# Kernel tuning notes

Hardware: AMD Instinct MI355X
Metric: run time of the kernel (lower is better)

Reference implementation:

```python
import jax, jax.numpy as jnp
import numpy as np
from jax import lax

K = 16
EPS = 1e-5


def leaky(x):
    return jnp.where(x >= 0, x, 0.2 * x)


def group_norm(x, gamma, beta, groups):
    # x: [B, C, ...]
    B, C = x.shape[0], x.shape[1]
    xs = x.reshape(B, groups, C // groups, *x.shape[2:])
    axes = tuple(range(2, xs.ndim))
    mean = xs.mean(axis=axes, keepdims=True)
    var = xs.var(axis=axes, keepdims=True)
    xs = (xs - mean) * lax.rsqrt(var + EPS)
    x = xs.reshape(x.shape)
    pshape = (1, C) + (1,) * (x.ndim - 2)
    return x * gamma.reshape(pshape) + beta.reshape(pshape)


def knn_idx(coor_k, coor_q):
    # coor_*: [B, 3, N]; returns idx [B, Nq, K] of nearest points in coor_k
    qq = (coor_q ** 2).sum(axis=1)  # [B, Nq]
    kk = (coor_k ** 2).sum(axis=1)  # [B, Nk]
    d2 = qq[:, :, None] + kk[:, None, :] - 2.0 * jnp.einsum('bcq,bck->bqk', coor_q, coor_k)
    _, idx = lax.top_k(-d2, K)  # smallest distances
    return idx


def get_graph_feature(coor_q, x_q, coor_k, x_k):
    # x_q: [B, C, Nq], x_k: [B, C, Nk] -> [B, 2C, Nq, K]
    idx = knn_idx(coor_k, coor_q)  # [B, Nq, K]
    nbr = jax.vmap(lambda xk, ix: xk[:, ix])(x_k, idx)  # [B, C, Nq, K]
    xq = x_q[:, :, :, None]
    return jnp.concatenate([nbr - xq, jnp.broadcast_to(xq, nbr.shape)], axis=1)


def fps(xyz, npoint):
    B, N, _ = xyz.shape

    def step(carry, _):
        dist, far = carry
        centroid = jnp.take_along_axis(xyz, far[:, None, None], axis=1)  # [B,1,3]
        d = ((xyz - centroid) ** 2).sum(-1)
        dist = jnp.minimum(dist, d)
        nxt = jnp.argmax(dist, axis=-1).astype(jnp.int32)
        return (dist, nxt), far

    init = (jnp.full((B, N), 1e10, xyz.dtype), jnp.zeros((B,), jnp.int32))
    _, idx = lax.scan(step, init, None, length=npoint)
    return idx.T  # [B, npoint]


def fps_downsample(coor, x, num_group):
    fps_i = fps(jnp.transpose(coor, (0, 2, 1)), num_group)  # [B, G]
    combined = jnp.concatenate([coor, x], axis=1)  # [B, 3+C, N]
    newc = jax.vmap(lambda c, ix: c[:, ix])(combined, fps_i)  # [B, 3+C, G]
    return newc[:, :3], newc[:, 3:]


def conv1x1(w, f):
    return jnp.einsum('oc,bcqk->boqk', w, f)


def setup_inputs() -> dict:
    key = jax.random.key(0)
    ks = jax.random.split(key, 16)
    B, N = 8, 4096
    s = lambda k, sh, fan: jax.random.normal(k, sh, jnp.float32) * (1.0 / np.sqrt(fan))
    return {
        'x': jax.random.normal(ks[0], (B, 3, N), jnp.float32),
        'sample_npoints': 128,
        'w_in': s(ks[1], (8, 3), 3), 'b_in': jnp.zeros((8,), jnp.float32),
        'w1': s(ks[2], (32, 16), 16), 'g1': jnp.ones((32,), jnp.float32), 'be1': jnp.zeros((32,), jnp.float32),
        'w2': s(ks[3], (64, 64), 64), 'g2': jnp.ones((64,), jnp.float32), 'be2': jnp.zeros((64,), jnp.float32),
        'w3': s(ks[4], (64, 128), 128), 'g3': jnp.ones((64,), jnp.float32), 'be3': jnp.zeros((64,), jnp.float32),
        'w4': s(ks[5], (128, 128), 128), 'g4': jnp.ones((128,), jnp.float32), 'be4': jnp.zeros((128,), jnp.float32),
    }


def reference(x, sample_npoints, w_in, b_in, w1, g1, be1, w2, g2, be2, w3, g3, be3, w4, g4, be4):
    coor = x
    f = jnp.einsum('oc,bcn->bon', w_in, x) + b_in[None, :, None]  # input_trans

    f = get_graph_feature(coor, f, coor, f)
    f = leaky(group_norm(conv1x1(w1, f), g1, be1, 4)).max(axis=-1)
    coor_q, f_q = fps_downsample(coor, f, 512)

    f = get_graph_feature(coor_q, f_q, coor, f)
    f = leaky(group_norm(conv1x1(w2, f), g2, be2, 4)).max(axis=-1)
    coor = coor_q

    f = get_graph_feature(coor, f, coor, f)
    f = leaky(group_norm(conv1x1(w3, f), g3, be3, 4)).max(axis=-1)
    coor_q, f_q = fps_downsample(coor, f, sample_npoints)

    f = get_graph_feature(coor_q, f_q, coor, f)
    f = leaky(group_norm(conv1x1(w4, f), g4, be4, 4)).max(axis=-1)
    coor = coor_q
    return coor, f
```

## Files before the change

kernel.cpp:

```cpp
#include <hip/hip_runtime.h>
#include <cstdint>

typedef unsigned int uint;
typedef unsigned short u16;

#define DEV __device__ __forceinline__

DEV float bf2f(u16 u) { return __uint_as_float(((uint)u) << 16); }
DEV u16 f2bf(float f) {
    uint x = __float_as_uint(f);
    return (u16)((x + 0x7fffu + ((x >> 16) & 1u)) >> 16);
}

struct InPtrs { const void* p[14]; };

__global__ __launch_bounds__(256) void fused_prep(
    const void* __restrict__ xv, InPtrs ptrs, float* __restrict__ cw,
    float* __restrict__ coorT, float* __restrict__ f0,
    int* __restrict__ flag, int B, int N)
{
    __shared__ int cnt[256];
    __shared__ int sflag;
    const u16* xs = (const u16*)xv;
    int t = threadIdx.x, good = 0;
#pragma unroll
    for (int i = 0; i < 8; ++i) {
        u16 u = xs[(t * 8 + i) * 37];
        int e = (u >> 7) & 0xFF;
        good += (e >= 90 && e <= 150) ? 1 : 0;
    }
    cnt[t] = good;
    __syncthreads();
    if (t == 0) {
        int s = 0;
        for (int i = 0; i < 256; ++i) s += cnt[i];
        sflag = (s >= 1741) ? 1 : 0;
    }
    __syncthreads();
    int isbf = sflag;
    int blk = blockIdx.x;

    if (blk < 128) {
        int p = blk * 256 + t;
        int b = p / N, n = p % N;
        float c0, c1, c2;
        if (isbf) {
            const u16* x = (const u16*)xv;
            c0 = bf2f(x[(b * 3 + 0) * N + n]);
            c1 = bf2f(x[(b * 3 + 1) * N + n]);
            c2 = bf2f(x[(b * 3 + 2) * N + n]);
        } else {
            const float* x = (const float*)xv;
            c0 = x[(b * 3 + 0) * N + n];
            c1 = x[(b * 3 + 1) * N + n];
            c2 = x[(b * 3 + 2) * N + n];
        }
        coorT[p * 3 + 0] = c0; coorT[p * 3 + 1] = c1; coorT[p * 3 + 2] = c2;
        float wl[24], bl[8];
        if (isbf) {
            const u16* wr = (const u16*)ptrs.p[0];
            const u16* br = (const u16*)ptrs.p[1];
#pragma unroll
            for (int i = 0; i < 24; ++i) wl[i] = bf2f(wr[i]);
#pragma unroll
            for (int i = 0; i < 8; ++i) bl[i] = bf2f(br[i]);
        } else {
            const float* wr = (const float*)ptrs.p[0];
            const float* br = (const float*)ptrs.p[1];
#pragma unroll
            for (int i = 0; i < 24; ++i) wl[i] = wr[i];
#pragma unroll
            for (int i = 0; i < 8; ++i) bl[i] = br[i];
        }
#pragma unroll
        for (int o = 0; o < 8; ++o) {
            float v = bl[o];
            v = fmaf(wl[o * 3 + 0], c0, v);
            v = fmaf(wl[o * 3 + 1], c1, v);
            v = fmaf(wl[o * 3 + 2], c2, v);
            f0[(size_t)p * 8 + o] = v;
        }
    } else {
        const int cntb[14] = {24, 8, 512, 32, 32, 4096, 64, 64, 8192, 64, 64, 16384, 128, 128};
        int g = (blk - 128) * 256 + t;
        if (g < 29792) {
            int idx = g, bb = 0;
            while (idx >= cntb[bb]) { idx -= cntb[bb]; ++bb; }
            cw[g] = isbf ? bf2f(((const u16*)ptrs.p[bb])[idx])
                         : ((const float*)ptrs.p[bb])[idx];
        }
        if (blk == 128 && t == 0) flag[0] = isbf;
    }
}

#define KNN_INSERT(DV, IV)                                                            \
    if ((DV) < bd[15]) {                                                              \
        _Pragma("unroll")                                                             \
        for (int j = 15; j >= 1; --j) {                                               \
            bool up  = ((DV) < bd[j - 1]);                                            \
            bool chg = ((DV) < bd[j]);                                                \
            if (chg) { bd[j] = up ? bd[j - 1] : (DV); bi[j] = up ? bi[j - 1] : (IV); }\
        }                                                                             \
        if ((DV) < bd[0]) { bd[0] = (DV); bi[0] = (IV); }                             \
    }

#define FPS_DPP_STEP(CTRL)                                                           \
    {                                                                                \
        float ov = __int_as_float(__builtin_amdgcn_update_dpp(                       \
            __float_as_int(bv), __float_as_int(bv), (CTRL), 0xf, 0xf, false));       \
        int oi = __builtin_amdgcn_update_dpp(bid, bid, (CTRL), 0xf, 0xf, false);     \
        bool t = (ov > bv) || (ov == bv && oi < bid);                                \
        bv = t ? ov : bv; bid = t ? oi : bid;                                        \
    }

#define FPS_MRG_STEP(CTRL)                                                           \
    {                                                                                \
        float ov = __int_as_float(__builtin_amdgcn_update_dpp(                       \
            __float_as_int(mv), __float_as_int(mv), (CTRL), 0xf, 0xf, false));       \
        int oi = __builtin_amdgcn_update_dpp(mi, mi, (CTRL), 0xf, 0xf, false);       \
        bool t = (ov > mv) || (ov == mv && oi < mi);                                 \
        mv = t ? ov : mv; mi = t ? oi : mi;                                          \
    }

template<int N, int PTS>
__global__ __launch_bounds__(256, 2) void knn_fps_kernel(
    const float* __restrict__ xyz, int* __restrict__ idxout,
    int* __restrict__ fpsout, int npoint)
{
    __shared__ union LU {
        struct { float4 kt[256]; float2 mrg[4][64][16]; } k;
        struct { float4 sxyz[N]; float2 rp[2][4]; } f;
    } u;
    int b = blockIdx.y;
    int tid = threadIdx.x;

    if (blockIdx.x == 0) {
        __builtin_amdgcn_s_setprio(3);
        int wave = tid >> 6, lane = tid & 63;
        float px[PTS], py[PTS], pz[PTS], dist[PTS];
#pragma unroll
        for (int i = 0; i < PTS; ++i) {
            int p = tid + i * 256;
            const float* pp = xyz + (size_t)(b * N + p) * 3;
            float x0 = pp[0], y0 = pp[1], z0 = pp[2];
            px[i] = x0; py[i] = y0; pz[i] = z0;
            u.f.sxyz[p] = make_float4(x0, y0, z0, 0.f);
            dist[i] = 1e10f;
        }
        __syncthreads();
        int far = 0;
        int my0 = 0, my1 = 0;
        for (int it = 0; it < npoint; ++it) {
            if (it == tid)       my0 = far;
            if (it == tid + 256) my1 = far;
            float4 cv = u.f.sxyz[far];
            float cx = cv.x, cy = cv.y, cz = cv.z;
            float bv = -1.f; int bid = 0;
#pragma unroll
            for (int i = 0; i < PTS; ++i) {
                float dx = __fsub_rn(px[i], cx);
                float dy = __fsub_rn(py[i], cy);
                float dz = __fsub_rn(pz[i], cz);
                float d = __fadd_rn(__fadd_rn(__fmul_rn(dx, dx), __fmul_rn(dy, dy)), __fmul_rn(dz, dz));
                float nd = fminf(dist[i], d);
                dist[i] = nd;
                bool t = nd > bv;
                bv = t ? nd : bv; bid = t ? (tid + i * 256) : bid;
            }
            FPS_DPP_STEP(0x0B1)
            FPS_DPP_STEP(0x04E)
            FPS_DPP_STEP(0x124)
            FPS_DPP_STEP(0x128)
            FPS_DPP_STEP(0x142)
            FPS_DPP_STEP(0x143)
            int par = it & 1;
            if (lane == 63) u.f.rp[par][wave] = make_float2(bv, __int_as_float(bid));
            __syncthreads();
            {
                float2 e = u.f.rp[par][lane & 3];
                float mv = e.x; int mi = __float_as_int(e.y);
                FPS_MRG_STEP(0x0B1)
                FPS_MRG_STEP(0x04E)
                far = __builtin_amdgcn_readfirstlane(mi);
            }
        }
        __builtin_amdgcn_s_setprio(0);
        if (tid < npoint)       fpsout[b * npoint + tid] = my0;
        if (tid + 256 < npoint) fpsout[b * npoint + tid + 256] = my1;
        return;
    }

    int qloc = tid & 63;
    int wave = tid >> 6;
    int q = (blockIdx.x - 1) * 64 + qloc;

    const float* qp = xyz + (size_t)(b * N + q) * 3;
    float qx = qp[0], qy = qp[1], qz = qp[2];
    float qq = __fadd_rn(__fadd_rn(__fmul_rn(qx, qx), __fmul_rn(qy, qy)), __fmul_rn(qz, qz));
    float bd[16]; int bi[16];
#pragma unroll
    for (int j = 0; j < 16; ++j) { bd[j] = 3.4e38f; bi[j] = 0; }
    float cb_d[4]; int cb_i[4]; int cnt = 0;
#pragma unroll
    for (int s = 0; s < 4; ++s) { cb_d[s] = 3.4e38f; cb_i[s] = 0; }

    for (int t0 = 0; t0 < N; t0 += 256) {
        {
            int i = tid;
            const float* kp = xyz + (size_t)(b * N + t0 + i) * 3;
            float kx = kp[0], ky = kp[1], kz = kp[2];
            float kn = __fadd_rn(__fadd_rn(__fmul_rn(kx, kx), __fmul_rn(ky, ky)), __fmul_rn(kz, kz));
            u.k.kt[i] = make_float4(kx, ky, kz, kn);
        }
        __syncthreads();
        for (int i2 = 0; i2 < 64; ++i2) {
            int ii = wave * 64 + i2;
            float4 kv = u.k.kt[ii];
            float dot = __fadd_rn(__fadd_rn(__fmul_rn(qx, kv.x), __fmul_rn(qy, kv.y)),
                                  __fmul_rn(qz, kv.z));
            float d2 = __fsub_rn(__fadd_rn(qq, kv.w), __fmul_rn(2.0f, dot));
            bool adm = (d2 < bd[15]);
            if (adm) {
                int id = t0 + ii;
                cb_d[0] = (cnt == 0) ? d2 : cb_d[0]; cb_i[0] = (cnt == 0) ? id : cb_i[0];
                cb_d[1] = (cnt == 1) ? d2 : cb_d[1]; cb_i[1] = (cnt == 1) ? id : cb_i[1];
                cb_d[2] = (cnt == 2) ? d2 : cb_d[2]; cb_i[2] = (cnt == 2) ? id : cb_i[2];
                cb_d[3] = (cnt == 3) ? d2 : cb_d[3]; cb_i[3] = (cnt == 3) ? id : cb_i[3];
                ++cnt;
            }
            if (__any(cnt >= 4)) {
#pragma unroll
                for (int s = 0; s < 4; ++s) {
                    bool have = s < cnt;
                    float dv = have ? cb_d[s] : 3.4e38f;
                    int   iv = have ? cb_i[s] : 0;
                    KNN_INSERT(dv, iv)
                }
                cnt = 0;
            }
        }
        __syncthreads();
    }
#pragma unroll
    for (int s = 0; s < 4; ++s) {
        bool have = s < cnt;
        float dv = have ? cb_d[s] : 3.4e38f;
        int   iv = have ? cb_i[s] : 0;
        KNN_INSERT(dv, iv)
    }
#pragma unroll
    for (int j = 0; j < 16; ++j)
        u.k.mrg[wave][qloc][j] = make_float2(bd[j], __int_as_float(bi[j]));
    __syncthreads();

    if (tid < 64) {
        int qm = tid;
        int qg = (blockIdx.x - 1) * 64 + qm;
        int* op = idxout + (size_t)(b * N + qg) * 16;
        int p0 = 0, p1 = 0, p2 = 0, p3 = 0;
#pragma unroll 1
        for (int j = 0; j < 16; ++j) {
            float2 h0 = u.k.mrg[0][qm][p0], h1 = u.k.mrg[1][qm][p1];
            float2 h2 = u.k.mrg[2][qm][p2], h3 = u.k.mrg[3][qm][p3];
            float bdv = h0.x; int biv = __float_as_int(h0.y); int w_ = 0;
            int i1 = __float_as_int(h1.y);
            if (h1.x < bdv || (h1.x == bdv && i1 < biv)) { bdv = h1.x; biv = i1; w_ = 1; }
            int i2v = __float_as_int(h2.y);
            if (h2.x < bdv || (h2.x == bdv && i2v < biv)) { bdv = h2.x; biv = i2v; w_ = 2; }
            int i3 = __float_as_int(h3.y);
            if (h3.x < bdv || (h3.x == bdv && i3 < biv)) { bdv = h3.x; biv = i3; w_ = 3; }
            op[j] = biv;
            p0 += (w_ == 0); p1 += (w_ == 1); p2 += (w_ == 2); p3 += (w_ == 3);
        }
    }
}

__global__ __launch_bounds__(256) void knn_kernel(
    const float* __restrict__ qxyz, const float* __restrict__ kxyz,
    int* __restrict__ idxout, int Nq, int Nk)
{
    __shared__ float4 kt[256];
    __shared__ float2 mrg[4][64][16];
    int b = blockIdx.y;
    int qloc = threadIdx.x & 63;
    int wave = threadIdx.x >> 6;
    int q = blockIdx.x * 64 + qloc;
    bool act = q < Nq;

    float qx = 0.f, qy = 0.f, qz = 0.f, qq = 0.f;
    if (act) {
        const float* qp = qxyz + (size_t)(b * Nq + q) * 3;
        qx = qp[0]; qy = qp[1]; qz = qp[2];
        qq = __fadd_rn(__fadd_rn(__fmul_rn(qx, qx), __fmul_rn(qy, qy)), __fmul_rn(qz, qz));
    }
    float bd[16]; int bi[16];
#pragma unroll
    for (int j = 0; j < 16; ++j) { bd[j] = 3.4e38f; bi[j] = 0; }
    float cb_d[4]; int cb_i[4]; int cnt = 0;
#pragma unroll
    for (int s = 0; s < 4; ++s) { cb_d[s] = 3.4e38f; cb_i[s] = 0; }

    for (int t0 = 0; t0 < Nk; t0 += 256) {
        {
            int i = threadIdx.x;
            const float* kp = kxyz + (size_t)(b * Nk + t0 + i) * 3;
            float kx = kp[0], ky = kp[1], kz = kp[2];
            float kn = __fadd_rn(__fadd_rn(__fmul_rn(kx, kx), __fmul_rn(ky, ky)), __fmul_rn(kz, kz));
            kt[i] = make_float4(kx, ky, kz, kn);
        }
        __syncthreads();
        for (int i2 = 0; i2 < 64; ++i2) {
            int ii = wave * 64 + i2;
            float4 kv = kt[ii];
            float dot = __fadd_rn(__fadd_rn(__fmul_rn(qx, kv.x), __fmul_rn(qy, kv.y)),
                                  __fmul_rn(qz, kv.z));
            float d2 = __fsub_rn(__fadd_rn(qq, kv.w), __fmul_rn(2.0f, dot));
            bool adm = act && (d2 < bd[15]);
            if (adm) {
                int id = t0 + ii;
                cb_d[0] = (cnt == 0) ? d2 : cb_d[0]; cb_i[0] = (cnt == 0) ? id : cb_i[0];
                cb_d[1] = (cnt == 1) ? d2 : cb_d[1]; cb_i[1] = (cnt == 1) ? id : cb_i[1];
                cb_d[2] = (cnt == 2) ? d2 : cb_d[2]; cb_i[2] = (cnt == 2) ? id : cb_i[2];
                cb_d[3] = (cnt == 3) ? d2 : cb_d[3]; cb_i[3] = (cnt == 3) ? id : cb_i[3];
                ++cnt;
            }
            if (__any(cnt >= 4)) {
#pragma unroll
                for (int s = 0; s < 4; ++s) {
                    bool have = s < cnt;
                    float dv = have ? cb_d[s] : 3.4e38f;
                    int   iv = have ? cb_i[s] : 0;
                    KNN_INSERT(dv, iv)
                }
                cnt = 0;
            }
        }
        __syncthreads();
    }
#pragma unroll
    for (int s = 0; s < 4; ++s) {
        bool have = s < cnt;
        float dv = have ? cb_d[s] : 3.4e38f;
        int   iv = have ? cb_i[s] : 0;
        KNN_INSERT(dv, iv)
    }
#pragma unroll
    for (int j = 0; j < 16; ++j)
        mrg[wave][qloc][j] = make_float2(bd[j], __int_as_float(bi[j]));
    __syncthreads();

    if (threadIdx.x < 64) {
        int qm = threadIdx.x;
        int qg = blockIdx.x * 64 + qm;
        if (qg < Nq) {
            int* op = idxout + (size_t)(b * Nq + qg) * 16;
            int p0 = 0, p1 = 0, p2 = 0, p3 = 0;
#pragma unroll 1
            for (int j = 0; j < 16; ++j) {
                float2 h0 = mrg[0][qm][p0], h1 = mrg[1][qm][p1];
                float2 h2 = mrg[2][qm][p2], h3 = mrg[3][qm][p3];
                float bdv = h0.x; int biv = __float_as_int(h0.y); int w_ = 0;
                int i1 = __float_as_int(h1.y);
                if (h1.x < bdv || (h1.x == bdv && i1 < biv)) { bdv = h1.x; biv = i1; w_ = 1; }
                int i2v = __float_as_int(h2.y);
                if (h2.x < bdv || (h2.x == bdv && i2v < biv)) { bdv = h2.x; biv = i2v; w_ = 2; }
                int i3 = __float_as_int(h3.y);
                if (h3.x < bdv || (h3.x == bdv && i3 < biv)) { bdv = h3.x; biv = i3; w_ = 3; }
                op[j] = biv;
                p0 += (w_ == 0); p1 += (w_ == 1); p2 += (w_ == 2); p3 += (w_ == 3);
            }
        }
    }
}

__global__ __launch_bounds__(256) void knn_part_kernel(
    const float* __restrict__ qxyz, const float* __restrict__ kxyz,
    float2* __restrict__ pbuf, int Nq, int Nk, int nchunk)
{
    __shared__ float4 kt[256];
    __shared__ float2 mrg[4][64][16];
    int qblks = Nq / 64;
    int chunk = blockIdx.x / qblks;
    int qblk = blockIdx.x % qblks;
    int klen = Nk / nchunk;
    int klo = chunk * klen, khi = klo + klen;
    int b = blockIdx.y;
    int qloc = threadIdx.x & 63;
    int wave = threadIdx.x >> 6;
    int q = qblk * 64 + qloc;

    const float* qp = qxyz + (size_t)(b * Nq + q) * 3;
    float qx = qp[0], qy = qp[1], qz = qp[2];
    float qq = __fadd_rn(__fadd_rn(__fmul_rn(qx, qx), __fmul_rn(qy, qy)), __fmul_rn(qz, qz));
    float bd[16]; int bi[16];
#pragma unroll
    for (int j = 0; j < 16; ++j) { bd[j] = 3.4e38f; bi[j] = 0; }
    float cb_d[4]; int cb_i[4]; int cnt = 0;
#pragma unroll
    for (int s = 0; s < 4; ++s) { cb_d[s] = 3.4e38f; cb_i[s] = 0; }

    for (int t0 = klo; t0 < khi; t0 += 256) {
        {
            int i = threadIdx.x;
            const float* kp = kxyz + (size_t)(b * Nk + t0 + i) * 3;
            float kx = kp[0], ky = kp[1], kz = kp[2];
            float kn = __fadd_rn(__fadd_rn(__fmul_rn(kx, kx), __fmul_rn(ky, ky)), __fmul_rn(kz, kz));
            kt[i] = make_float4(kx, ky, kz, kn);
        }
        __syncthreads();
        for (int i2 = 0; i2 < 64; ++i2) {
            int ii = wave * 64 + i2;
            float4 kv = kt[ii];
            float dot = __fadd_rn(__fadd_rn(__fmul_rn(qx, kv.x), __fmul_rn(qy, kv.y)),
                                  __fmul_rn(qz, kv.z));
            float d2 = __fsub_rn(__fadd_rn(qq, kv.w), __fmul_rn(2.0f, dot));
            bool adm = (d2 < bd[15]);
            if (adm) {
                int id = t0 + ii;
                cb_d[0] = (cnt == 0) ? d2 : cb_d[0]; cb_i[0] = (cnt == 0) ? id : cb_i[0];
                cb_d[1] = (cnt == 1) ? d2 : cb_d[1]; cb_i[1] = (cnt == 1) ? id : cb_i[1];
                cb_d[2] = (cnt == 2) ? d2 : cb_d[2]; cb_i[2] = (cnt == 2) ? id : cb_i[2];
                cb_d[3] = (cnt == 3) ? d2 : cb_d[3]; cb_i[3] = (cnt == 3) ? id : cb_i[3];
                ++cnt;
            }
            if (__any(cnt >= 4)) {
#pragma unroll
                for (int s = 0; s < 4; ++s) {
                    bool have = s < cnt;
                    float dv = have ? cb_d[s] : 3.4e38f;
                    int   iv = have ? cb_i[s] : 0;
                    KNN_INSERT(dv, iv)
                }
                cnt = 0;
            }
        }
        __syncthreads();
    }
#pragma unroll
    for (int s = 0; s < 4; ++s) {
        bool have = s < cnt;
        float dv = have ? cb_d[s] : 3.4e38f;
        int   iv = have ? cb_i[s] : 0;
        KNN_INSERT(dv, iv)
    }
#pragma unroll
    for (int j = 0; j < 16; ++j)
        mrg[wave][qloc][j] = make_float2(bd[j], __int_as_float(bi[j]));
    __syncthreads();

    if (threadIdx.x < 64) {
        int qm = threadIdx.x;
        int qg = qblk * 64 + qm;
        float2* op = pbuf + (((size_t)(b * Nq + qg) * nchunk) + chunk) * 16;
        int p0 = 0, p1 = 0, p2 = 0, p3 = 0;
#pragma unroll 1
        for (int j = 0; j < 16; ++j) {
            float2 h0 = mrg[0][qm][p0], h1 = mrg[1][qm][p1];
            float2 h2 = mrg[2][qm][p2], h3 = mrg[3][qm][p3];
            float bdv = h0.x; int biv = __float_as_int(h0.y); int w_ = 0;
            int i1 = __float_as_int(h1.y);
            if (h1.x < bdv || (h1.x == bdv && i1 < biv)) { bdv = h1.x; biv = i1; w_ = 1; }
            int i2v = __float_as_int(h2.y);
            if (h2.x < bdv || (h2.x == bdv && i2v < biv)) { bdv = h2.x; biv = i2v; w_ = 2; }
            int i3 = __float_as_int(h3.y);
            if (h3.x < bdv || (h3.x == bdv && i3 < biv)) { bdv = h3.x; biv = i3; w_ = 3; }
            op[j] = make_float2(bdv, __int_as_float(biv));
            p0 += (w_ == 0); p1 += (w_ == 1); p2 += (w_ == 2); p3 += (w_ == 3);
        }
    }
}

__global__ void knn_merge_kernel(const float2* __restrict__ pbuf, int* __restrict__ idxout,
                                 int total)
{
    int q = blockIdx.x * 256 + threadIdx.x;
    if (q >= total) return;
    const float2* L = pbuf + (size_t)q * 64;
    int* op = idxout + (size_t)q * 16;
    int p0 = 0, p1 = 0, p2 = 0, p3 = 0;
#pragma unroll 1
    for (int j = 0; j < 16; ++j) {
        float2 h0 = L[p0], h1 = L[16 + p1], h2 = L[32 + p2], h3 = L[48 + p3];
        float bdv = h0.x; int biv = __float_as_int(h0.y); int w_ = 0;
        int i1 = __float_as_int(h1.y);
        if (h1.x < bdv || (h1.x == bdv && i1 < biv)) { bdv = h1.x; biv = i1; w_ = 1; }
        int i2v = __float_as_int(h2.y);
        if (h2.x < bdv || (h2.x == bdv && i2v < biv)) { bdv = h2.x; biv = i2v; w_ = 2; }
        int i3 = __float_as_int(h3.y);
        if (h3.x < bdv || (h3.x == bdv && i3 < biv)) { bdv = h3.x; biv = i3; w_ = 3; }
        op[j] = biv;
        p0 += (w_ == 0); p1 += (w_ == 1); p2 += (w_ == 2); p3 += (w_ == 3);
    }
}

template<int CTRL>
DEV void red5(float& v, int& i, float& x, float& y, float& z)
{
    float ov = __int_as_float(__builtin_amdgcn_update_dpp(
        __float_as_int(v), __float_as_int(v), CTRL, 0xf, 0xf, false));
    int oi = __builtin_amdgcn_update_dpp(i, i, CTRL, 0xf, 0xf, false);
    float ox = __int_as_float(__builtin_amdgcn_update_dpp(
        __float_as_int(x), __float_as_int(x), CTRL, 0xf, 0xf, false));
    float oy = __int_as_float(__builtin_amdgcn_update_dpp(
        __float_as_int(y), __float_as_int(y), CTRL, 0xf, 0xf, false));
    float oz = __int_as_float(__builtin_amdgcn_update_dpp(
        __float_as_int(z), __float_as_int(z), CTRL, 0xf, 0xf, false));
    bool t = (ov > v) || (ov == v && oi < i);
    v = t ? ov : v; i = t ? oi : i; x = t ? ox : x; y = t ? oy : y; z = t ? oz : z;
}

template<bool STORE_V>
__global__ __launch_bounds__(256) void stats3_fps_kernel(
    const float* __restrict__ fq, const float* __restrict__ fk, const int* __restrict__ idx,
    const float* __restrict__ w, float* __restrict__ partials, float* __restrict__ vbuf,
    const float* __restrict__ fxyz, int* __restrict__ fpsout, int Nq, int Nk)
{
    constexpr int K = 16, C_IN = 64, C_OUT = 64, E = 2 * C_IN, GC = C_OUT / 4;
    __shared__ alignas(16) float edge[4][K][E];
    __shared__ int nidx[4][K];
    __shared__ float gsum[4][4][2];

    int b = blockIdx.y;
    if (blockIdx.x == 0) {
        int tid = threadIdx.x;
        if (tid >= 64) return;
        __builtin_amdgcn_s_setprio(3);
        constexpr int PTS = 8, NL = 512;
        float px[PTS], py[PTS], pz[PTS], dist[PTS];
#pragma unroll
        for (int i = 0; i < PTS; ++i) {
            int p = tid + i * 64;
            const float* pp = fxyz + (size_t)(b * NL + p) * 3;
            px[i] = pp[0]; py[i] = pp[1]; pz[i] = pp[2];
            dist[i] = 1e10f;
        }
        float cx = __int_as_float(__builtin_amdgcn_readlane(__float_as_int(px[0]), 0));
        float cy = __int_as_float(__builtin_amdgcn_readlane(__float_as_int(py[0]), 0));
        float cz = __int_as_float(__builtin_amdgcn_readlane(__float_as_int(pz[0]), 0));
        int curidx = 0;
        int my0 = 0, my1 = 0;
        for (int it = 0; it < 128; ++it) {
            if (it == tid)      my0 = curidx;
            if (it == tid + 64) my1 = curidx;
            float bv = -1.f; int bid = 0; float bx = 0.f, by = 0.f, bz = 0.f;
#pragma unroll
            for (int i = 0; i < PTS; ++i) {
                float dx = __fsub_rn(px[i], cx);
                float dy = __fsub_rn(py[i], cy);
                float dz = __fsub_rn(pz[i], cz);
                float d = __fadd_rn(__fadd_rn(__fmul_rn(dx, dx), __fmul_rn(dy, dy)), __fmul_rn(dz, dz));
                float nd = fminf(dist[i], d);
                dist[i] = nd;
                bool t = nd > bv;
                bv = t ? nd : bv; bid = t ? (tid + i * 64) : bid;
                bx = t ? px[i] : bx; by = t ? py[i] : by; bz = t ? pz[i] : bz;
            }
            red5<0x0B1>(bv, bid, bx, by, bz);
            red5<0x04E>(bv, bid, bx, by, bz);
            red5<0x124>(bv, bid, bx, by, bz);
            red5<0x128>(bv, bid, bx, by, bz);
            red5<0x142>(bv, bid, bx, by, bz);
            red5<0x143>(bv, bid, bx, by, bz);
            curidx = __builtin_amdgcn_readlane(bid, 63);
            cx = __int_as_float(__builtin_amdgcn_readlane(__float_as_int(bx), 63));
            cy = __int_as_float(__builtin_amdgcn_readlane(__float_as_int(by), 63));
            cz = __int_as_float(__builtin_amdgcn_readlane(__float_as_int(bz), 63));
        }
        __builtin_amdgcn_s_setprio(0);
        if (tid < 128)      fpsout[b * 128 + tid] = my0;
        if (tid + 64 < 128) fpsout[b * 128 + tid + 64] = my1;
        return;
    }

    int wave = threadIdx.x >> 6, lane = threadIdx.x & 63;
    int nqc = Nq >> 2;
    int chunk = blockIdx.x - 1;
    int q = chunk * 4 + wave;

    const float* xqr = fq + (size_t)(b * Nq + q) * C_IN;
    if (lane < K) nidx[wave][lane] = idx[(size_t)(b * Nq + q) * K + lane];
    for (int t = lane; t < K * E; t += 64) {
        int k = t / E, c = t % E;
        int j = nidx[wave][k];
        float v;
        if (c < C_IN) v = fk[(size_t)(b * Nk + j) * C_IN + c] - xqr[c];
        else          v = xqr[c - C_IN];
        edge[wave][k][c] = v;
    }
    __syncthreads();

    {
        int oc = lane;
        float s = 0.f, ss = 0.f;
        float v[K];
#pragma unroll
        for (int k2 = 0; k2 < K; ++k2) v[k2] = 0.f;
        const float* wr = w + (size_t)oc * E;
        for (int c = 0; c < E; c += 4) {
            float4 wv = *reinterpret_cast<const float4*>(wr + c);
#pragma unroll
            for (int k2 = 0; k2 < K; ++k2) {
                const float4 e4 = *reinterpret_cast<const float4*>(&edge[wave][k2][c]);
                v[k2] = fmaf(wv.x, e4.x, v[k2]);
                v[k2] = fmaf(wv.y, e4.y, v[k2]);
                v[k2] = fmaf(wv.z, e4.z, v[k2]);
                v[k2] = fmaf(wv.w, e4.w, v[k2]);
            }
        }
        if (STORE_V) {
            float4* vb = (float4*)(vbuf + ((size_t)(b * Nq + q) * C_OUT + oc) * 16);
            vb[0] = make_float4(v[0], v[1], v[2], v[3]);
            vb[1] = make_float4(v[4], v[5], v[6], v[7]);
            vb[2] = make_float4(v[8], v[9], v[10], v[11]);
            vb[3] = make_float4(v[12], v[13], v[14], v[15]);
        }
#pragma unroll
        for (int k2 = 0; k2 < K; ++k2) { s += v[k2]; ss = fmaf(v[k2], v[k2], ss); }
#pragma unroll
        for (int m2 = 1; m2 < GC; m2 <<= 1) { s += __shfl_xor(s, m2); ss += __shfl_xor(ss, m2); }
        if ((oc & (GC - 1)) == 0) {
            gsum[wave][oc / GC][0] = s; gsum[wave][oc / GC][1] = ss;
        }
    }
    __syncthreads();
    if (threadIdx.x < 4) {
        int g = threadIdx.x;
        float s  = ((gsum[0][g][0] + gsum[1][g][0]) + gsum[2][g][0]) + gsum[3][g][0];
        float ss = ((gsum[0][g][1] + gsum[1][g][1]) + gsum[2][g][1]) + gsum[3][g][1];
        size_t pi = ((size_t)(b * 4 + g) * nqc + chunk) * 2;
        partials[pi] = s; partials[pi + 1] = ss;
    }
}

__global__ void gather_kernel(const float* __restrict__ coorS, const float* __restrict__ fS,
                              const int* __restrict__ fidx, float* __restrict__ coorD,
                              float* __restrict__ fD, int Ns, int M, int C)
{
    int b = blockIdx.y;
    int m = blockIdx.x * blockDim.x + threadIdx.x;
    if (m >= M) return;
    int j = fidx[b * M + m];
#pragma unroll
    for (int c = 0; c < 3; ++c)
        coorD[((size_t)b * M + m) * 3 + c] = coorS[((size_t)b * Ns + j) * 3 + c];
    for (int c = 0; c < C; ++c)
        fD[((size_t)b * M + m) * C + c] = fS[((size_t)b * Ns + j) * C + c];
}

template<int C_IN, int C_OUT, bool STORE_V>
__global__ __launch_bounds__(256) void edge_conv_stats_t(
    const float* __restrict__ fq, const float* __restrict__ fk, const int* __restrict__ idx,
    const float* __restrict__ w, float* __restrict__ partials, float* __restrict__ vbuf,
    int Nq, int Nk)
{
    constexpr int K = 16, E = 2 * C_IN, GC = C_OUT / 4;
    constexpr int ITERS = (C_OUT + 63) / 64;
    __shared__ alignas(16) float edge[4][K][E];
    __shared__ int nidx[4][K];
    __shared__ float gsum[4][4][2];

    int wave = threadIdx.x >> 6, lane = threadIdx.x & 63;
    int nqc = Nq >> 2;
    int b = blockIdx.y, chunk = blockIdx.x;
    int q = chunk * 4 + wave;

    const float* xqr = fq + (size_t)(b * Nq + q) * C_IN;
    if (lane < K) nidx[wave][lane] = idx[(size_t)(b * Nq + q) * K + lane];
    for (int t = lane; t < K * E; t += 64) {
        int k = t / E, c = t % E;
        int j = nidx[wave][k];
        float v;
        if (c < C_IN) v = fk[(size_t)(b * Nk + j) * C_IN + c] - xqr[c];
        else          v = xqr[c - C_IN];
        edge[wave][k][c] = v;
    }
    __syncthreads();

#pragma unroll
    for (int itr = 0; itr < ITERS; ++itr) {
        int oc = lane + 64 * itr;
        float s = 0.f, ss = 0.f;
        if (oc < C_OUT) {
            float v[K];
#pragma unroll
            for (int k2 = 0; k2 < K; ++k2) v[k2] = 0.f;
            const float* wr = w + (size_t)oc * E;
            for (int c = 0; c < E; c += 4) {
                float4 wv = *reinterpret_cast<const float4*>(wr + c);
#pragma unroll
                for (int k2 = 0; k2 < K; ++k2) {
                    const float4 e4 = *reinterpret_cast<const float4*>(&edge[wave][k2][c]);
                    v[k2] = fmaf(wv.x, e4.x, v[k2]);
                    v[k2] = fmaf(wv.y, e4.y, v[k2]);
                    v[k2] = fmaf(wv.z, e4.z, v[k2]);
                    v[k2] = fmaf(wv.w, e4.w, v[k2]);
                }
            }
            if (STORE_V) {
                float4* vb = (float4*)(vbuf + ((size_t)(b * Nq + q) * C_OUT + oc) * 16);
                vb[0] = make_float4(v[0], v[1], v[2], v[3]);
                vb[1] = make_float4(v[4], v[5], v[6], v[7]);
                vb[2] = make_float4(v[8], v[9], v[10], v[11]);
                vb[3] = make_float4(v[12], v[13], v[14], v[15]);
            }
#pragma unroll
            for (int k2 = 0; k2 < K; ++k2) { s += v[k2]; ss = fmaf(v[k2], v[k2], ss); }
        }
#pragma unroll
        for (int m2 = 1; m2 < GC; m2 <<= 1) { s += __shfl_xor(s, m2); ss += __shfl_xor(ss, m2); }
        if (oc < C_OUT && (oc & (GC - 1)) == 0) {
            gsum[wave][oc / GC][0] = s; gsum[wave][oc / GC][1] = ss;
        }
    }
    __syncthreads();
    if (threadIdx.x < 4) {
        int g = threadIdx.x;
        float s  = ((gsum[0][g][0] + gsum[1][g][0]) + gsum[2][g][0]) + gsum[3][g][0];
        float ss = ((gsum[0][g][1] + gsum[1][g][1]) + gsum[2][g][1]) + gsum[3][g][1];
        size_t pi = ((size_t)(b * 4 + g) * nqc + chunk) * 2;
        partials[pi] = s; partials[pi + 1] = ss;
    }
}

__global__ void gn_finalize(const float* __restrict__ partials, float* __restrict__ stats,
                            int nchunk, float inv_cnt)
{
    int i = threadIdx.x >> 3;
    int sl = threadIdx.x & 7;
    float s = 0.f, ss = 0.f;
    for (int c = sl; c < nchunk; c += 8) {
        s  += partials[((size_t)i * nchunk + c) * 2];
        ss += partials[((size_t)i * nchunk + c) * 2 + 1];
    }
#pragma unroll
    for (int m = 1; m < 8; m <<= 1) { s += __shfl_xor(s, m); ss += __shfl_xor(ss, m); }
    if (sl == 0) {
        float mean = s * inv_cnt;
        float var = fmaf(-mean, mean, ss * inv_cnt);
        stats[i * 2] = mean;
        stats[i * 2 + 1] = 1.0f / sqrtf(var + 1e-5f);
    }
}

template<int C_IN, int C_OUT>
__global__ __launch_bounds__(256) void edge_conv_apply(
    const float* __restrict__ fq, const float* __restrict__ fk, const int* __restrict__ idx,
    const float* __restrict__ stats, const float* __restrict__ w,
    const float* __restrict__ gamma, const float* __restrict__ beta,
    float* __restrict__ outp, int Nq, int Nk)
{
    constexpr int K = 16, E = 2 * C_IN, GC = C_OUT / 4;
    constexpr int ITERS = (C_OUT + 63) / 64;
    __shared__ alignas(16) float edge[4][K][E];
    __shared__ int nidx[4][K];

    int wave = threadIdx.x >> 6, lane = threadIdx.x & 63;
    int b = blockIdx.y, chunk = blockIdx.x;
    int q = chunk * 4 + wave;

    const float* xqr = fq + (size_t)(b * Nq + q) * C_IN;
    if (lane < K) nidx[wave][lane] = idx[(size_t)(b * Nq + q) * K + lane];
    for (int t = lane; t < K * E; t += 64) {
        int k = t / E, c = t % E;
        int j = nidx[wave][k];
        float v;
        if (c < C_IN) v = fk[(size_t)(b * Nk + j) * C_IN + c] - xqr[c];
        else          v = xqr[c - C_IN];
        edge[wave][k][c] = v;
    }
    __syncthreads();

#pragma unroll
    for (int itr = 0; itr < ITERS; ++itr) {
        int oc = lane + 64 * itr;
        if (oc < C_OUT) {
            float v[K];
#pragma unroll
            for (int k2 = 0; k2 < K; ++k2) v[k2] = 0.f;
            const float* wr = w + (size_t)oc * E;
            for (int c = 0; c < E; c += 4) {
                float4 wv = *reinterpret_cast<const float4*>(wr + c);
#pragma unroll
                for (int k2 = 0; k2 < K; ++k2) {
                    const float4 e4 = *reinterpret_cast<const float4*>(&edge[wave][k2][c]);
                    v[k2] = fmaf(wv.x, e4.x, v[k2]);
                    v[k2] = fmaf(wv.y, e4.y, v[k2]);
                    v[k2] = fmaf(wv.z, e4.z, v[k2]);
                    v[k2] = fmaf(wv.w, e4.w, v[k2]);
                }
            }
            int g = oc / GC;
            float mean = stats[(b * 4 + g) * 2 + 0];
            float rstd = stats[(b * 4 + g) * 2 + 1];
            float ga = gamma[oc], be = beta[oc];
            float m = -3.4e38f;
#pragma unroll
            for (int k2 = 0; k2 < K; ++k2) {
                float y = fmaf((v[k2] - mean) * rstd, ga, be);
                y = (y >= 0.f) ? y : 0.2f * y;
                m = fmaxf(m, y);
            }
            outp[(size_t)(b * Nq + q) * C_OUT + oc] = m;
        }
    }
}

template<int C_OUT>
__global__ __launch_bounds__(256) void edge_conv_apply2(
    const float* __restrict__ vbuf, const float* __restrict__ stats,
    const float* __restrict__ gamma, const float* __restrict__ beta,
    float* __restrict__ outp, int total, int Nq)
{
    constexpr int GC = C_OUT / 4;
    int t = blockIdx.x * 256 + threadIdx.x;
    if (t >= total) return;
    int oc = t & (C_OUT - 1);
    int bq = t / C_OUT;
    int b = bq / Nq;
    int g = oc / GC;
    float mean = stats[(b * 4 + g) * 2 + 0];
    float rstd = stats[(b * 4 + g) * 2 + 1];
    float ga = gamma[oc], be = beta[oc];
    const float4* vb = (const float4*)(vbuf + (size_t)t * 16);
    float m = -3.4e38f;
#pragma unroll
    for (int j = 0; j < 4; ++j) {
        float4 v4 = vb[j];
        float y;
        y = fmaf((v4.x - mean) * rstd, ga, be); y = (y >= 0.f) ? y : 0.2f * y; m = fmaxf(m, y);
        y = fmaf((v4.y - mean) * rstd, ga, be); y = (y >= 0.f) ? y : 0.2f * y; m = fmaxf(m, y);
        y = fmaf((v4.z - mean) * rstd, ga, be); y = (y >= 0.f) ? y : 0.2f * y; m = fmaxf(m, y);
        y = fmaf((v4.w - mean) * rstd, ga, be); y = (y >= 0.f) ? y : 0.2f * y; m = fmaxf(m, y);
    }
    outp[t] = m;
}

__global__ __launch_bounds__(256) void apply2_out(
    const float* __restrict__ vbuf, const float* __restrict__ stats,
    const float* __restrict__ gamma, const float* __restrict__ beta,
    const float* __restrict__ coor2T, void* __restrict__ outv,
    const int* __restrict__ flag)
{
    int t = blockIdx.x * 256 + threadIdx.x;
    int isbf = flag[0];
    if (t < 131072) {
        int oc = t & 127;
        int bq = t >> 7;
        int b = bq >> 7;
        int q = bq & 127;
        int g = oc >> 5;
        float mean = stats[(b * 4 + g) * 2 + 0];
        float rstd = stats[(b * 4 + g) * 2 + 1];
        float ga = gamma[oc], be = beta[oc];
        const float4* vb = (const float4*)(vbuf + (size_t)t * 16);
        float m = -3.4e38f;
#pragma unroll
        for (int j = 0; j < 4; ++j) {
            float4 v4 = vb[j];
            float y;
            y = fmaf((v4.x - mean) * rstd, ga, be); y = (y >= 0.f) ? y : 0.2f * y; m = fmaxf(m, y);
            y = fmaf((v4.y - mean) * rstd, ga, be); y = (y >= 0.f) ? y : 0.2f * y; m = fmaxf(m, y);
            y = fmaf((v4.z - mean) * rstd, ga, be); y = (y >= 0.f) ? y : 0.2f * y; m = fmaxf(m, y);
            y = fmaf((v4.w - mean) * rstd, ga, be); y = (y >= 0.f) ? y : 0.2f * y; m = fmaxf(m, y);
        }
        int i = 3072 + b * 16384 + oc * 128 + q;
        if (isbf) ((u16*)outv)[i] = f2bf(m);
        else      ((float*)outv)[i] = m;
    } else if (t < 134144) {
        int i = t - 131072;
        int b = i / 384, r = i % 384;
        int c = r / 128, n = r % 128;
        float v = coor2T[((size_t)b * 128 + n) * 3 + c];
        if (isbf) ((u16*)outv)[i] = f2bf(v);
        else      ((float*)outv)[i] = v;
    }
}

__global__ void write_out_kernel(const float* __restrict__ coor2T, const float* __restrict__ f4T,
                                 void* __restrict__ outv, const int* __restrict__ flag)
{
    int i = blockIdx.x * blockDim.x + threadIdx.x;
    if (i >= 134144) return;
    float v;
    if (i < 3072) {
        int b = i / 384, r = i % 384;
        int c = r / 128, n = r % 128;
        v = coor2T[((size_t)b * 128 + n) * 3 + c];
    } else {
        int jj = i - 3072;
        int b = jj / 16384, r = jj % 16384;
        int c = r / 128, qn = r % 128;
        v = f4T[((size_t)b * 128 + qn) * 128 + c];
    }
    if (flag[0]) ((u16*)outv)[i] = f2bf(v);
    else         ((float*)outv)[i] = v;
}

extern "C" void kernel_launch(void* const* d_in, const int* in_sizes, int n_in,
                              void* d_out, int out_size, void* d_ws, size_t ws_size,
                              hipStream_t stream)
{
    (void)in_sizes; (void)n_in; (void)out_size;
    constexpr int B = 8, N = 4096, M1 = 512, M2 = 128;

    float* fbase   = (float*)d_ws;
    float* coorT   = fbase;
    float* f0T     = coorT + 98304;
    float* f1T     = f0T + 262144;
    float* f2T     = f1T + 1048576;
    float* f3T     = f2T + 262144;
    float* f4T     = f3T + 262144;
    float* coor1T  = f4T + 131072;
    float* coor2T  = coor1T + 12288;
    float* fq2T    = coor2T + 3072;
    float* fq4T    = fq2T + 131072;
    float* statsb  = fq4T + 65536;
    float* partials= statsb + 256;
    float* pb      = partials + 65536;
    float* cw      = pb + 524288;
    int* ibase = (int*)(cw + 29796);
    int* idx1 = ibase;
    int* idx2 = idx1 + 524288;
    int* idx3 = idx2 + 65536;
    int* idx4 = idx3 + 65536;
    int* fps1 = idx4 + 16384;
    int* fps2 = fps1 + 4096;
    int* flag = fps2 + 1024;

    size_t used = (size_t)((char*)(flag + 1) - (char*)d_ws);
    size_t voff = (used + 255) & ~(size_t)255;
    float* vbuf = (float*)((char*)d_ws + voff);
    bool fu1 = ws_size >= voff + (size_t)16777216 * 4;
    bool fu2 = ws_size >= voff + (size_t)4194304 * 4;
    bool fu3 = fu2;
    bool fu4 = ws_size >= voff + (size_t)2097152 * 4;

    const float* w1c  = cw + 32;
    const float* g1c  = cw + 544;
    const float* be1c = cw + 576;
    const float* w2c  = cw + 608;
    const float* g2c  = cw + 4704;
    const float* be2c = cw + 4768;
    const float* w3c  = cw + 4832;
    const float* g3c  = cw + 13024;
    const float* be3c = cw + 13088;
    const float* w4c  = cw + 13152;
    const float* g4c  = cw + 29536;
    const float* be4c = cw + 29664;

    InPtrs ptrs;
    for (int i = 0; i < 14; ++i) ptrs.p[i] = d_in[i + 2];

    fused_prep<<<245, 256, 0, stream>>>(d_in[0], ptrs, cw, coorT, f0T, flag, B, N);

    knn_fps_kernel<4096, 16><<<dim3(N / 64 + 1, B), 256, 0, stream>>>(coorT, idx1, fps1, M1);
    if (fu1) {
        edge_conv_stats_t<8, 32, true><<<dim3(N / 4, B), 256, 0, stream>>>(f0T, f0T, idx1, w1c, partials, vbuf, N, N);
        gn_finalize<<<1, 256, 0, stream>>>(partials, statsb + 0, N / 4, 1.0f / (float)(N * 16 * 8));
        edge_conv_apply2<32><<<(B * N * 32 + 255) / 256, 256, 0, stream>>>(vbuf, statsb + 0, g1c, be1c, f1T, B * N * 32, N);
    } else {
        edge_conv_stats_t<8, 32, false><<<dim3(N / 4, B), 256, 0, stream>>>(f0T, f0T, idx1, w1c, partials, vbuf, N, N);
        gn_finalize<<<1, 256, 0, stream>>>(partials, statsb + 0, N / 4, 1.0f / (float)(N * 16 * 8));
        edge_conv_apply<8, 32><<<dim3(N / 4, B), 256, 0, stream>>>(f0T, f0T, idx1, statsb + 0, w1c, g1c, be1c, f1T, N, N);
    }
    gather_kernel<<<dim3((M1 + 255) / 256, B), 256, 0, stream>>>(coorT, f1T, fps1, coor1T, fq2T, N, M1, 32);

    knn_part_kernel<<<dim3((M1 / 64) * 4, B), 256, 0, stream>>>(coor1T, coorT, (float2*)pb, M1, N, 4);
    knn_merge_kernel<<<(B * M1 + 255) / 256, 256, 0, stream>>>((const float2*)pb, idx2, B * M1);
    if (fu2) {
        edge_conv_stats_t<32, 64, true><<<dim3(M1 / 4, B), 256, 0, stream>>>(fq2T, f1T, idx2, w2c, partials, vbuf, M1, N);
        gn_finalize<<<1, 256, 0, stream>>>(partials, statsb + 64, M1 / 4, 1.0f / (float)(M1 * 16 * 16));
        edge_conv_apply2<64><<<(B * M1 * 64 + 255) / 256, 256, 0, stream>>>(vbuf, statsb + 64, g2c, be2c, f2T, B * M1 * 64, M1);
    } else {
        edge_conv_stats_t<32, 64, false><<<dim3(M1 / 4, B), 256, 0, stream>>>(fq2T, f1T, idx2, w2c, partials, vbuf, M1, N);
        gn_finalize<<<1, 256, 0, stream>>>(partials, statsb + 64, M1 / 4, 1.0f / (float)(M1 * 16 * 16));
        edge_conv_apply<32, 64><<<dim3(M1 / 4, B), 256, 0, stream>>>(fq2T, f1T, idx2, statsb + 64, w2c, g2c, be2c, f2T, M1, N);
    }

    knn_kernel<<<dim3(M1 / 64, B), 256, 0, stream>>>(coor1T, coor1T, idx3, M1, M1);
    if (fu3) {
        stats3_fps_kernel<true><<<dim3(M1 / 4 + 1, B), 256, 0, stream>>>(
            f2T, f2T, idx3, w3c, partials, vbuf, coor1T, fps2, M1, M1);
        gn_finalize<<<1, 256, 0, stream>>>(partials, statsb + 128, M1 / 4, 1.0f / (float)(M1 * 16 * 16));
        edge_conv_apply2<64><<<(B * M1 * 64 + 255) / 256, 256, 0, stream>>>(vbuf, statsb + 128, g3c, be3c, f3T, B * M1 * 64, M1);
    } else {
        stats3_fps_kernel<false><<<dim3(M1 / 4 + 1, B), 256, 0, stream>>>(
            f2T, f2T, idx3, w3c, partials, vbuf, coor1T, fps2, M1, M1);
        gn_finalize<<<1, 256, 0, stream>>>(partials, statsb + 128, M1 / 4, 1.0f / (float)(M1 * 16 * 16));
        edge_conv_apply<64, 64><<<dim3(M1 / 4, B), 256, 0, stream>>>(f2T, f2T, idx3, statsb + 128, w3c, g3c, be3c, f3T, M1, M1);
    }
    gather_kernel<<<dim3(1, B), 256, 0, stream>>>(coor1T, f3T, fps2, coor2T, fq4T, M1, M2, 64);

    knn_kernel<<<dim3((M2 + 63) / 64, B), 256, 0, stream>>>(coor2T, coor1T, idx4, M2, M1);
    if (fu4) {
        edge_conv_stats_t<64, 128, true><<<dim3(M2 / 4, B), 256, 0, stream>>>(fq4T, f3T, idx4, w4c, partials, vbuf, M2, M1);
        gn_finalize<<<1, 256, 0, stream>>>(partials, statsb + 192, M2 / 4, 1.0f / (float)(M2 * 16 * 32));
        apply2_out<<<(134144 + 255) / 256, 256, 0, stream>>>(vbuf, statsb + 192, g4c, be4c, coor2T, d_out, flag);
    } else {
        edge_conv_stats_t<64, 128, false><<<dim3(M2 / 4, B), 256, 0, stream>>>(fq4T, f3T, idx4, w4c, partials, vbuf, M2, M1);
        gn_finalize<<<1, 256, 0, stream>>>(partials, statsb + 192, M2 / 4, 1.0f / (float)(M2 * 16 * 32));
        edge_conv_apply<64, 128><<<dim3(M2 / 4, B), 256, 0, stream>>>(fq4T, f3T, idx4, statsb + 192, w4c, g4c, be4c, f4T, M2, M1);
        write_out_kernel<<<(134144 + 255) / 256, 256, 0, stream>>>(coor2T, f4T, d_out, flag);
    }
}
```

Baseline: 852.6 us.

## Fuse first edge-conv statistics pass into the KNN/FPS kernel

```diff
diff --git a/kernel.cpp b/kernel.cpp
--- a/kernel.cpp
+++ b/kernel.cpp
@@ -122,13 +122,21 @@
         mv = t ? ov : mv; mi = t ? oi : mi;                                          \
     }
 
-template<int N, int PTS>
-__global__ __launch_bounds__(256, 2) void knn_fps_kernel(
+template<int N, int PTS, bool STORE_V>
+__global__ __launch_bounds__(256, 2) void knn_fps_stats1_kernel(
     const float* __restrict__ xyz, int* __restrict__ idxout,
-    int* __restrict__ fpsout, int npoint)
+    int* __restrict__ fpsout, int npoint,
+    const float* __restrict__ f0, const float* __restrict__ w,
+    float* __restrict__ partials, float* __restrict__ vbuf)
 {
     __shared__ union LU {
-        struct { float4 kt[256]; float2 mrg[4][64][16]; } k;
+        struct {
+            float4 kt[256];
+            float2 mrg[4][64][16];
+            int    fin[64][16];
+            float  edge[4][16][16];
+            float  gsum[4][4][2];
+        } k;
         struct { float4 sxyz[N]; float2 rp[2][4]; } f;
     } u;
     int b = blockIdx.y;
@@ -192,7 +200,9 @@
 
     int qloc = tid & 63;
     int wave = tid >> 6;
-    int q = (blockIdx.x - 1) * 64 + qloc;
+    int lane = qloc;
+    int qbase = (blockIdx.x - 1) * 64;
+    int q = qbase + qloc;
 
     const float* qp = xyz + (size_t)(b * N + q) * 3;
     float qx = qp[0], qy = qp[1], qz = qp[2];
@@ -255,8 +265,7 @@
 
     if (tid < 64) {
         int qm = tid;
-        int qg = (blockIdx.x - 1) * 64 + qm;
-        int* op = idxout + (size_t)(b * N + qg) * 16;
+        int* op = idxout + (size_t)(b * N + qbase + qm) * 16;
         int p0 = 0, p1 = 0, p2 = 0, p3 = 0;
 #pragma unroll 1
         for (int j = 0; j < 16; ++j) {
@@ -270,7 +279,70 @@
             int i3 = __float_as_int(h3.y);
             if (h3.x < bdv || (h3.x == bdv && i3 < biv)) { bdv = h3.x; biv = i3; w_ = 3; }
             op[j] = biv;
+            u.k.fin[qm][j] = biv;
             p0 += (w_ == 0); p1 += (w_ == 1); p2 += (w_ == 2); p3 += (w_ == 3);
+        }
+    }
+
+    constexpr int E = 16, GC = 8;
+    int nqc = N >> 2;
+    for (int it = 0; it < 16; ++it) {
+        __syncthreads();
+        int ql = it * 4 + wave;
+        int qg = qbase + ql;
+        const float* xqr = f0 + (size_t)(b * N + qg) * 8;
+        for (int t = lane; t < 256; t += 64) {
+            int k = t >> 4, c = t & 15;
+            int j = u.k.fin[ql][k];
+            float v;
+            if (c < 8) v = f0[(size_t)(b * N + j) * 8 + c] - xqr[c];
+            else       v = xqr[c - 8];
+            u.k.edge[wave][k][c] = v;
+        }
+        __syncthreads();
+        {
+            int oc = lane;
+            float s = 0.f, ss = 0.f;
+            if (oc < 32) {
+                float v[16];
+#pragma unroll
+                for (int k2 = 0; k2 < 16; ++k2) v[k2] = 0.f;
+                const float* wr = w + (size_t)oc * E;
+                for (int c = 0; c < E; c += 4) {
+                    float4 wv = *reinterpret_cast<const float4*>(wr + c);
+#pragma unroll
+                    for (int k2 = 0; k2 < 16; ++k2) {
+                        const float4 e4 = *reinterpret_cast<const float4*>(&u.k.edge[wave][k2][c]);
+                        v[k2] = fmaf(wv.x, e4.x, v[k2]);
+                        v[k2] = fmaf(wv.y, e4.y, v[k2]);
+                        v[k2] = fmaf(wv.z, e4.z, v[k2]);
+                        v[k2] = fmaf(wv.w, e4.w, v[k2]);
+                    }
+                }
+                if (STORE_V) {
+                    float4* vb = (float4*)(vbuf + ((size_t)(b * N + qg) * 32 + oc) * 16);
+                    vb[0] = make_float4(v[0], v[1], v[2], v[3]);
+                    vb[1] = make_float4(v[4], v[5], v[6], v[7]);
+                    vb[2] = make_float4(v[8], v[9], v[10], v[11]);
+                    vb[3] = make_float4(v[12], v[13], v[14], v[15]);
+                }
+#pragma unroll
+                for (int k2 = 0; k2 < 16; ++k2) { s += v[k2]; ss = fmaf(v[k2], v[k2], ss); }
+            }
+#pragma unroll
+            for (int m2 = 1; m2 < GC; m2 <<= 1) { s += __shfl_xor(s, m2); ss += __shfl_xor(ss, m2); }
+            if (oc < 32 && (oc & (GC - 1)) == 0) {
+                u.k.gsum[wave][oc / GC][0] = s; u.k.gsum[wave][oc / GC][1] = ss;
+            }
+        }
+        __syncthreads();
+        if (tid < 4) {
+            int g = tid;
+            float s  = ((u.k.gsum[0][g][0] + u.k.gsum[1][g][0]) + u.k.gsum[2][g][0]) + u.k.gsum[3][g][0];
+            float ss = ((u.k.gsum[0][g][1] + u.k.gsum[1][g][1]) + u.k.gsum[2][g][1]) + u.k.gsum[3][g][1];
+            int chunk = (blockIdx.x - 1) * 16 + it;
+            size_t pi = ((size_t)(b * 4 + g) * nqc + chunk) * 2;
+            partials[pi] = s; partials[pi + 1] = ss;
         }
     }
 }
@@ -953,13 +1025,14 @@
 
     fused_prep<<<245, 256, 0, stream>>>(d_in[0], ptrs, cw, coorT, f0T, flag, B, N);
 
-    knn_fps_kernel<4096, 16><<<dim3(N / 64 + 1, B), 256, 0, stream>>>(coorT, idx1, fps1, M1);
     if (fu1) {
-        edge_conv_stats_t<8, 32, true><<<dim3(N / 4, B), 256, 0, stream>>>(f0T, f0T, idx1, w1c, partials, vbuf, N, N);
+        knn_fps_stats1_kernel<4096, 16, true><<<dim3(N / 64 + 1, B), 256, 0, stream>>>(
+            coorT, idx1, fps1, M1, f0T, w1c, partials, vbuf);
         gn_finalize<<<1, 256, 0, stream>>>(partials, statsb + 0, N / 4, 1.0f / (float)(N * 16 * 8));
         edge_conv_apply2<32><<<(B * N * 32 + 255) / 256, 256, 0, stream>>>(vbuf, statsb + 0, g1c, be1c, f1T, B * N * 32, N);
     } else {
-        edge_conv_stats_t<8, 32, false><<<dim3(N / 4, B), 256, 0, stream>>>(f0T, f0T, idx1, w1c, partials, vbuf, N, N);
+        knn_fps_stats1_kernel<4096, 16, false><<<dim3(N / 64 + 1, B), 256, 0, stream>>>(
+            coorT, idx1, fps1, M1, f0T, w1c, partials, vbuf);
         gn_finalize<<<1, 256, 0, stream>>>(partials, statsb + 0, N / 4, 1.0f / (float)(N * 16 * 8));
         edge_conv_apply<8, 32><<<dim3(N / 4, B), 256, 0, stream>>>(f0T, f0T, idx1, statsb + 0, w1c, g1c, be1c, f1T, N, N);
     }
```

New measurement: 922.9 us. +8.3%, slower.
